# Kernel tuning notes

Measured on AMD Instinct MI355X. Metric: run time of the kernel, lower is better.

## Reference

```python
import jax, jax.numpy as jnp
import numpy as np
import math

HIDDEN = 128

def setup_inputs() -> dict:
    key = jax.random.key(0)
    k1, k2, k3 = jax.random.split(key, 3)
    X = jax.random.normal(k1, (4, 4096, HIDDEN), dtype=jnp.float32)
    # nn.Linear(hidden, 3*hidden): weight [3H, H], bias [3H]
    bound = 1.0 / math.sqrt(HIDDEN)
    W = jax.random.uniform(k2, (3 * HIDDEN, HIDDEN), minval=-bound, maxval=bound, dtype=jnp.float32)
    b = jax.random.uniform(k3, (3 * HIDDEN,), minval=-bound, maxval=bound, dtype=jnp.float32)
    return {"X": X, "W": W, "b": b}

def reference(X, W, b):
    H = X.shape[-1]
    # fused QKV projection: X @ W^T + b -> [B, S, 3H]
    qkv = jnp.einsum('bsh,oh->bso', X, W) + b
    Q, K, V = jnp.split(qkv, 3, axis=-1)
    # scaled dot-product attention (single head)
    scores = jnp.einsum('bqh,bkh->bqk', Q, K) / jnp.sqrt(jnp.asarray(H, X.dtype))
    weights = jax.nn.softmax(scores, axis=-1)
    return jnp.einsum('bqk,bkh->bqh', weights, V)
```

## Files before the change

kernel.cpp:

```cpp
#include <hip/hip_runtime.h>
#include <hip/hip_fp16.h>

typedef _Float16 f16;
typedef __attribute__((ext_vector_type(8))) _Float16 f16x8;
typedef __attribute__((ext_vector_type(4))) float f32x4;
typedef __attribute__((ext_vector_type(4))) unsigned int u32x4;
typedef __attribute__((ext_vector_type(2))) unsigned int u32x2;

#define BB 4
#define SS 4096
#define HH 128
#define SC2 0.12752462157076558f
#define M2  5.7707801635558535f

union H2U { __half2 h; unsigned int u; };
union VU { u32x4 v; unsigned short s[8]; };
union F8U { u32x4 u; f16x8 h; };

__global__ __launch_bounds__(256, 2) void qkv_gemm(
    const float* __restrict__ X, const float* __restrict__ W,
    const float* __restrict__ bias, f16* __restrict__ Qh,
    f16* __restrict__ Kh, f16* __restrict__ Vh)
{
    const int bid = blockIdx.x;
    const int t = threadIdx.x;
    const int w = t >> 6, lane = t & 63;
    const int c = lane & 15, quad = lane >> 4;
    const int rbase = bid * 32;

    f16x8 wf[6][4];
#pragma unroll
    for (int mt = 0; mt < 6; ++mt) {
        const float* wr = W + (size_t)(w * 96 + mt * 16 + c) * HH + quad * 8;
#pragma unroll
        for (int kc = 0; kc < 4; ++kc) {
            float4 a = *(const float4*)(wr + kc * 32);
            float4 b = *(const float4*)(wr + kc * 32 + 4);
            H2U u0, u1, u2, u3;
            u0.h = __floats2half2_rn(a.x, a.y);
            u1.h = __floats2half2_rn(a.z, a.w);
            u2.h = __floats2half2_rn(b.x, b.y);
            u3.h = __floats2half2_rn(b.z, b.w);
            F8U pk; pk.u.x = u0.u; pk.u.y = u1.u; pk.u.z = u2.u; pk.u.w = u3.u;
            wf[mt][kc] = pk.h;
        }
    }
    float4 bb[6];
#pragma unroll
    for (int mt = 0; mt < 6; ++mt)
        bb[mt] = *(const float4*)&bias[w * 96 + mt * 16 + quad * 4];

#pragma unroll
    for (int nt = 0; nt < 2; ++nt) {
        f16x8 xf[4];
        const float* xr = X + (size_t)(rbase + nt * 16 + c) * HH + quad * 8;
#pragma unroll
        for (int kc = 0; kc < 4; ++kc) {
            float4 a = *(const float4*)(xr + kc * 32);
            float4 b = *(const float4*)(xr + kc * 32 + 4);
            H2U u0, u1, u2, u3;
            u0.h = __floats2half2_rn(a.x, a.y);
            u1.h = __floats2half2_rn(a.z, a.w);
            u2.h = __floats2half2_rn(b.x, b.y);
            u3.h = __floats2half2_rn(b.z, b.w);
            F8U pk; pk.u.x = u0.u; pk.u.y = u1.u; pk.u.z = u2.u; pk.u.w = u3.u;
            xf[kc] = pk.h;
        }
        f32x4 acc[6];
#pragma unroll
        for (int mt = 0; mt < 6; ++mt) acc[mt] = (f32x4)0.f;
#pragma unroll
        for (int kc = 0; kc < 4; ++kc)
#pragma unroll
            for (int mt = 0; mt < 6; ++mt)
                acc[mt] = __builtin_amdgcn_mfma_f32_16x16x32_f16(wf[mt][kc], xf[kc], acc[mt], 0, 0, 0);

        const int xrow = rbase + nt * 16 + c;
#pragma unroll
        for (int mt = 0; mt < 6; ++mt) {
            const int gcol = w * 96 + mt * 16;
            const int seg = gcol >> 7;
            const int cc = (gcol & 127) + quad * 4;
            f16* dst = (seg == 0) ? Qh : (seg == 1) ? Kh : Vh;
            H2U h0, h1;
            h0.h = __floats2half2_rn(acc[mt][0] + bb[mt].x, acc[mt][1] + bb[mt].y);
            h1.h = __floats2half2_rn(acc[mt][2] + bb[mt].z, acc[mt][3] + bb[mt].w);
            u32x2 pk; pk.x = h0.u; pk.y = h1.u;
            *(u32x2*)(dst + (size_t)xrow * HH + cc) = pk;
        }
    }
}

#define BM 128
#define BN 64
#define LK 136
#define LV 72
#define LP 40

__global__ __launch_bounds__(256, 2) void attn_mfma(
    const f16* __restrict__ Qh, const f16* __restrict__ Kh,
    const f16* __restrict__ Vh, float* __restrict__ out,
    float* __restrict__ Opart, float* __restrict__ l_arr, int nsplit)
{
    __shared__ f16 sK[BN * LK];
    __shared__ f16 sVt[HH * LV];
    __shared__ f16 sP[4][32 * LP];

    const int bid = blockIdx.x;
    const int split = bid >> 7;
    const int inner = bid & 127;
    const int batch = inner & 3;
    const int qtile = inner >> 2;
    const int t = threadIdx.x;
    const int w = t >> 6, lane = t & 63;
    const int c = lane & 15, quad = lane >> 4;

    const int s0 = (64 * split) / nsplit;
    const int s1 = (64 * (split + 1)) / nsplit;
    const int nst = s1 - s0;
    const int kstart = s0 * BN;

    const f16* Qb = Qh + (size_t)batch * SS * HH;
    const f16* Kb = Kh + (size_t)batch * SS * HH;
    const f16* Vb = Vh + (size_t)batch * SS * HH;
    const int qbase = qtile * BM + w * 32;

    f16x8 qf[2][4];
#pragma unroll
    for (int qt = 0; qt < 2; ++qt)
#pragma unroll
        for (int kc = 0; kc < 4; ++kc)
            qf[qt][kc] = *(const f16x8*)(Qb + (size_t)(qbase + qt * 16 + c) * HH + kc * 32 + quad * 8);

    const int kr = t >> 2, q4 = t & 3;
    const f16* kgp = Kb + (size_t)(kstart + kr) * HH + q4 * 32;
    f16* ksp = sK + kr * LK + q4 * 32;
    const int vkp = t & 31, vhq = t >> 5;
    const f16* vgp = Vb + (size_t)(kstart + 2 * vkp) * HH + vhq * 16;

    u32x4 kbuf[4], vb0[2], vb1[2];
#pragma unroll
    for (int i = 0; i < 4; ++i) kbuf[i] = *(const u32x4*)(kgp + i * 8);
#pragma unroll
    for (int i = 0; i < 2; ++i) {
        vb0[i] = *(const u32x4*)(vgp + i * 8);
        vb1[i] = *(const u32x4*)(vgp + HH + i * 8);
    }

    f32x4 oacc[2][8];
#pragma unroll
    for (int mt = 0; mt < 2; ++mt)
#pragma unroll
        for (int nt = 0; nt < 8; ++nt) oacc[mt][nt] = (f32x4)0.f;
    f32x4 oaccl[2];
    oaccl[0] = (f32x4)0.f; oaccl[1] = (f32x4)0.f;
    const f16x8 ones = {1, 1, 1, 1, 1, 1, 1, 1};

    for (int st = 0; st < nst; ++st) {
        __syncthreads();
#pragma unroll
        for (int i = 0; i < 4; ++i) *(u32x4*)(ksp + i * 8) = kbuf[i];
        {
            VU a0, a1, b0, b1;
            a0.v = vb0[0]; a1.v = vb0[1]; b0.v = vb1[0]; b1.v = vb1[1];
#pragma unroll
            for (int d = 0; d < 8; ++d) {
                unsigned int pk = (unsigned int)a0.s[d] | ((unsigned int)b0.s[d] << 16);
                *(unsigned int*)&sVt[(vhq * 16 + d) * LV + 2 * vkp] = pk;
            }
#pragma unroll
            for (int d = 0; d < 8; ++d) {
                unsigned int pk = (unsigned int)a1.s[d] | ((unsigned int)b1.s[d] << 16);
                *(unsigned int*)&sVt[(vhq * 16 + 8 + d) * LV + 2 * vkp] = pk;
            }
        }
        __syncthreads();
        if (st + 1 < nst) {
            const f16* kg = kgp + (size_t)(st + 1) * BN * HH;
#pragma unroll
            for (int i = 0; i < 4; ++i) kbuf[i] = *(const u32x4*)(kg + i * 8);
            const f16* vg = vgp + (size_t)(st + 1) * BN * HH;
#pragma unroll
            for (int i = 0; i < 2; ++i) {
                vb0[i] = *(const u32x4*)(vg + i * 8);
                vb1[i] = *(const u32x4*)(vg + HH + i * 8);
            }
        }

        f32x4 sacc[4][2];
#pragma unroll
        for (int km = 0; km < 4; ++km)
#pragma unroll
            for (int qt = 0; qt < 2; ++qt) sacc[km][qt] = (f32x4)0.f;
#pragma unroll
        for (int kc = 0; kc < 4; ++kc) {
#pragma unroll
            for (int km = 0; km < 4; ++km) {
                f16x8 kf = *(const f16x8*)&sK[(km * 16 + c) * LK + kc * 32 + quad * 8];
#pragma unroll
                for (int qt = 0; qt < 2; ++qt)
                    sacc[km][qt] = __builtin_amdgcn_mfma_f32_16x16x32_f16(kf, qf[qt][kc], sacc[km][qt], 0, 0, 0);
            }
        }

#pragma unroll
        for (int h = 0; h < 2; ++h) {
#pragma unroll
            for (int qt = 0; qt < 2; ++qt) {
#pragma unroll
                for (int km2 = 0; km2 < 2; ++km2) {
                    const int km = 2 * h + km2;
                    float p0 = exp2f(sacc[km][qt][0] * SC2 - M2);
                    float p1 = exp2f(sacc[km][qt][1] * SC2 - M2);
                    float p2 = exp2f(sacc[km][qt][2] * SC2 - M2);
                    float p3 = exp2f(sacc[km][qt][3] * SC2 - M2);
                    H2U u0, u1;
                    u0.h = __floats2half2_rn(p0, p1);
                    u1.h = __floats2half2_rn(p2, p3);
                    u32x2 pk; pk.x = u0.u; pk.y = u1.u;
                    *(u32x2*)&sP[w][(qt * 16 + c) * LP + km2 * 16 + quad * 4] = pk;
                }
            }
            f16x8 pf[2];
#pragma unroll
            for (int mt = 0; mt < 2; ++mt)
                pf[mt] = *(const f16x8*)&sP[w][(mt * 16 + c) * LP + quad * 8];
#pragma unroll
            for (int mt = 0; mt < 2; ++mt)
                oaccl[mt] = __builtin_amdgcn_mfma_f32_16x16x32_f16(pf[mt], ones, oaccl[mt], 0, 0, 0);
#pragma unroll
            for (int nt = 0; nt < 8; ++nt) {
                f16x8 vf = *(const f16x8*)&sVt[(nt * 16 + c) * LV + h * 32 + quad * 8];
#pragma unroll
                for (int mt = 0; mt < 2; ++mt)
                    oacc[mt][nt] = __builtin_amdgcn_mfma_f32_16x16x32_f16(pf[mt], vf, oacc[mt][nt], 0, 0, 0);
            }
        }
    }

    float* Ob = (split == 0) ? out : (Opart + (size_t)(split - 1) * BB * SS * HH);
    float* ob = Ob + (size_t)(batch * SS + qbase) * HH;
    if (nsplit == 1) {
#pragma unroll
        for (int mt = 0; mt < 2; ++mt) {
#pragma unroll
            for (int r = 0; r < 4; ++r) {
                const float lv = 1.f / oaccl[mt][r];
                const int row = mt * 16 + quad * 4 + r;
#pragma unroll
                for (int nt = 0; nt < 8; ++nt)
                    ob[(size_t)row * HH + nt * 16 + c] = oacc[mt][nt][r] * lv;
            }
        }
    } else {
#pragma unroll
        for (int mt = 0; mt < 2; ++mt) {
#pragma unroll
            for (int r = 0; r < 4; ++r) {
                const int row = mt * 16 + quad * 4 + r;
#pragma unroll
                for (int nt = 0; nt < 8; ++nt)
                    ob[(size_t)row * HH + nt * 16 + c] = oacc[mt][nt][r];
            }
        }
        if (c == 0) {
#pragma unroll
            for (int mt = 0; mt < 2; ++mt)
#pragma unroll
                for (int r = 0; r < 4; ++r)
                    l_arr[((size_t)split * BB + batch) * SS + qbase + mt * 16 + quad * 4 + r] = oaccl[mt][r];
        }
    }
}

__global__ __launch_bounds__(256) void attn_merge(
    float* __restrict__ out, const float* __restrict__ Opart,
    const float* __restrict__ l_arr, int nsplit)
{
    const int idx = blockIdx.x * 256 + threadIdx.x;
    const int chunk = idx & 31;
    const int q = (idx >> 5) & (SS - 1);
    const int b = idx >> 17;
    float L = 0.f;
    for (int s = 0; s < nsplit; ++s)
        L += l_arr[((size_t)s * BB + b) * SS + q];
    float4 a = *(const float4*)(out + ((size_t)b * SS + q) * HH + chunk * 4);
    for (int s = 1; s < nsplit; ++s) {
        const float* Op = Opart + (size_t)(s - 1) * BB * SS * HH;
        float4 o = *(const float4*)(Op + ((size_t)b * SS + q) * HH + chunk * 4);
        a.x += o.x; a.y += o.y; a.z += o.z; a.w += o.w;
    }
    const float inv = 1.f / L;
    a.x *= inv; a.y *= inv; a.z *= inv; a.w *= inv;
    *(float4*)(out + ((size_t)b * SS + q) * HH + chunk * 4) = a;
}

extern "C" void kernel_launch(void* const* d_in, const int* in_sizes, int n_in,
                              void* d_out, int out_size, void* d_ws, size_t ws_size,
                              hipStream_t stream) {
    const float* X = (const float*)d_in[0];
    const float* W = (const float*)d_in[1];
    const float* bias = (const float*)d_in[2];
    float* out = (float*)d_out;

    char* ws = (char*)d_ws;
    const size_t qkv_bytes = (size_t)3 * BB * SS * HH * sizeof(f16);
    const size_t o_bytes   = (size_t)BB * SS * HH * sizeof(float);
    const size_t l_bytes   = (size_t)BB * SS * sizeof(float);

    int S = 1;
    for (int cand = 4; cand >= 2; --cand) {
        if (ws_size >= qkv_bytes + (size_t)(cand - 1) * o_bytes + (size_t)cand * l_bytes) {
            S = cand; break;
        }
    }

    f16* Qh = (f16*)ws;
    f16* Kh = Qh + (size_t)BB * SS * HH;
    f16* Vh = Kh + (size_t)BB * SS * HH;
    float* Opart = (float*)(ws + qkv_bytes);
    float* l_arr = (float*)(ws + qkv_bytes + (size_t)(S - 1) * o_bytes);

    qkv_gemm<<<512, 256, 0, stream>>>(X, W, bias, Qh, Kh, Vh);
    attn_mfma<<<128 * S, 256, 0, stream>>>(Qh, Kh, Vh, out, Opart, l_arr, S);
    if (S > 1)
        attn_merge<<<BB * SS * (HH / 4) / 256, 256, 0, stream>>>(out, Opart, l_arr, S);
}
```

Baseline: 133.6 us.

## Pre-convert W to fp16, double GEMM rows per block, load K fragments directly

Adds a small kernel that converts W to fp16 once per call, so each qkv_gemm block loads half-precision weights instead of converting fp32. Each GEMM block now covers 64 rows instead of 32, halving the grid and the per-block weight loads. The attention kernel drops the shared-memory K tile and reads K MFMA fragments straight from global memory each step, and the V transpose staging is reorganised into wider 4-key packed LDS writes. This costs an extra launch and higher register pressure from the 16 K fragments, and loses K reuse across waves through LDS.

```diff
diff --git a/kernel.cpp b/kernel.cpp
--- a/kernel.cpp
+++ b/kernel.cpp
@@ -17,8 +17,20 @@
 union VU { u32x4 v; unsigned short s[8]; };
 union F8U { u32x4 u; f16x8 h; };
 
+__global__ __launch_bounds__(256) void wcvt(const float* __restrict__ W,
+                                            f16* __restrict__ Wh)
+{
+    const int idx = (blockIdx.x * 256 + threadIdx.x) * 4;
+    float4 v = *(const float4*)(W + idx);
+    H2U h0, h1;
+    h0.h = __floats2half2_rn(v.x, v.y);
+    h1.h = __floats2half2_rn(v.z, v.w);
+    u32x2 pk; pk.x = h0.u; pk.y = h1.u;
+    *(u32x2*)(Wh + idx) = pk;
+}
+
 __global__ __launch_bounds__(256, 2) void qkv_gemm(
-    const float* __restrict__ X, const float* __restrict__ W,
+    const float* __restrict__ X, const f16* __restrict__ Wh,
     const float* __restrict__ bias, f16* __restrict__ Qh,
     f16* __restrict__ Kh, f16* __restrict__ Vh)
 {
@@ -26,24 +38,15 @@
     const int t = threadIdx.x;
     const int w = t >> 6, lane = t & 63;
     const int c = lane & 15, quad = lane >> 4;
-    const int rbase = bid * 32;
+    const int rbase = bid * 64;
 
     f16x8 wf[6][4];
 #pragma unroll
     for (int mt = 0; mt < 6; ++mt) {
-        const float* wr = W + (size_t)(w * 96 + mt * 16 + c) * HH + quad * 8;
-#pragma unroll
-        for (int kc = 0; kc < 4; ++kc) {
-            float4 a = *(const float4*)(wr + kc * 32);
-            float4 b = *(const float4*)(wr + kc * 32 + 4);
-            H2U u0, u1, u2, u3;
-            u0.h = __floats2half2_rn(a.x, a.y);
-            u1.h = __floats2half2_rn(a.z, a.w);
-            u2.h = __floats2half2_rn(b.x, b.y);
-            u3.h = __floats2half2_rn(b.z, b.w);
-            F8U pk; pk.u.x = u0.u; pk.u.y = u1.u; pk.u.z = u2.u; pk.u.w = u3.u;
-            wf[mt][kc] = pk.h;
-        }
+        const f16* wr = Wh + (size_t)(w * 96 + mt * 16 + c) * HH + quad * 8;
+#pragma unroll
+        for (int kc = 0; kc < 4; ++kc)
+            wf[mt][kc] = *(const f16x8*)(wr + kc * 32);
     }
     float4 bb[6];
 #pragma unroll
@@ -51,7 +54,7 @@
         bb[mt] = *(const float4*)&bias[w * 96 + mt * 16 + quad * 4];
 
 #pragma unroll
-    for (int nt = 0; nt < 2; ++nt) {
+    for (int nt = 0; nt < 4; ++nt) {
         f16x8 xf[4];
         const float* xr = X + (size_t)(rbase + nt * 16 + c) * HH + quad * 8;
 #pragma unroll
@@ -93,7 +96,6 @@
 
 #define BM 128
 #define BN 64
-#define LK 136
 #define LV 72
 #define LP 40
 
@@ -102,7 +104,6 @@
     const f16* __restrict__ Vh, float* __restrict__ out,
     float* __restrict__ Opart, float* __restrict__ l_arr, int nsplit)
 {
-    __shared__ f16 sK[BN * LK];
     __shared__ f16 sVt[HH * LV];
     __shared__ f16 sP[4][32 * LP];
 
@@ -132,20 +133,15 @@
         for (int kc = 0; kc < 4; ++kc)
             qf[qt][kc] = *(const f16x8*)(Qb + (size_t)(qbase + qt * 16 + c) * HH + kc * 32 + quad * 8);
 
-    const int kr = t >> 2, q4 = t & 3;
-    const f16* kgp = Kb + (size_t)(kstart + kr) * HH + q4 * 32;
-    f16* ksp = sK + kr * LK + q4 * 32;
-    const int vkp = t & 31, vhq = t >> 5;
-    const f16* vgp = Vb + (size_t)(kstart + 2 * vkp) * HH + vhq * 16;
-
-    u32x4 kbuf[4], vb0[2], vb1[2];
-#pragma unroll
-    for (int i = 0; i < 4; ++i) kbuf[i] = *(const u32x4*)(kgp + i * 8);
-#pragma unroll
-    for (int i = 0; i < 2; ++i) {
-        vb0[i] = *(const u32x4*)(vgp + i * 8);
-        vb1[i] = *(const u32x4*)(vgp + HH + i * 8);
-    }
+    const int vk4 = t & 15;
+    const int vdg = t >> 4;
+    const f16* vgp = Vb + (size_t)(kstart + 4 * vk4) * HH + vdg * 8;
+
+    u32x4 vb[4];
+#pragma unroll
+    for (int j = 0; j < 4; ++j) vb[j] = *(const u32x4*)(vgp + (size_t)j * HH);
+
+    const f16* kfb = Kb + (size_t)(kstart + c) * HH + quad * 8;
 
     f32x4 oacc[2][8];
 #pragma unroll
@@ -157,34 +153,31 @@
     const f16x8 ones = {1, 1, 1, 1, 1, 1, 1, 1};
 
     for (int st = 0; st < nst; ++st) {
+        const f16* kst = kfb + (size_t)st * BN * HH;
+        f16x8 kf[4][4];
+#pragma unroll
+        for (int km = 0; km < 4; ++km)
+#pragma unroll
+            for (int kc = 0; kc < 4; ++kc)
+                kf[km][kc] = *(const f16x8*)(kst + (size_t)(km * 16) * HH + kc * 32);
+
         __syncthreads();
-#pragma unroll
-        for (int i = 0; i < 4; ++i) *(u32x4*)(ksp + i * 8) = kbuf[i];
         {
-            VU a0, a1, b0, b1;
-            a0.v = vb0[0]; a1.v = vb0[1]; b0.v = vb1[0]; b1.v = vb1[1];
+            VU u0, u1, u2, u3;
+            u0.v = vb[0]; u1.v = vb[1]; u2.v = vb[2]; u3.v = vb[3];
 #pragma unroll
             for (int d = 0; d < 8; ++d) {
-                unsigned int pk = (unsigned int)a0.s[d] | ((unsigned int)b0.s[d] << 16);
-                *(unsigned int*)&sVt[(vhq * 16 + d) * LV + 2 * vkp] = pk;
-            }
-#pragma unroll
-            for (int d = 0; d < 8; ++d) {
-                unsigned int pk = (unsigned int)a1.s[d] | ((unsigned int)b1.s[d] << 16);
-                *(unsigned int*)&sVt[(vhq * 16 + 8 + d) * LV + 2 * vkp] = pk;
+                u32x2 pk;
+                pk.x = (unsigned int)u0.s[d] | ((unsigned int)u1.s[d] << 16);
+                pk.y = (unsigned int)u2.s[d] | ((unsigned int)u3.s[d] << 16);
+                *(u32x2*)&sVt[(vdg * 8 + d) * LV + 4 * vk4] = pk;
             }
         }
         __syncthreads();
         if (st + 1 < nst) {
-            const f16* kg = kgp + (size_t)(st + 1) * BN * HH;
-#pragma unroll
-            for (int i = 0; i < 4; ++i) kbuf[i] = *(const u32x4*)(kg + i * 8);
             const f16* vg = vgp + (size_t)(st + 1) * BN * HH;
 #pragma unroll
-            for (int i = 0; i < 2; ++i) {
-                vb0[i] = *(const u32x4*)(vg + i * 8);
-                vb1[i] = *(const u32x4*)(vg + HH + i * 8);
-            }
+            for (int j = 0; j < 4; ++j) vb[j] = *(const u32x4*)(vg + (size_t)j * HH);
         }
 
         f32x4 sacc[4][2];
@@ -193,15 +186,12 @@
 #pragma unroll
             for (int qt = 0; qt < 2; ++qt) sacc[km][qt] = (f32x4)0.f;
 #pragma unroll
-        for (int kc = 0; kc < 4; ++kc) {
-#pragma unroll
-            for (int km = 0; km < 4; ++km) {
-                f16x8 kf = *(const f16x8*)&sK[(km * 16 + c) * LK + kc * 32 + quad * 8];
+        for (int kc = 0; kc < 4; ++kc)
+#pragma unroll
+            for (int km = 0; km < 4; ++km)
 #pragma unroll
                 for (int qt = 0; qt < 2; ++qt)
-                    sacc[km][qt] = __builtin_amdgcn_mfma_f32_16x16x32_f16(kf, qf[qt][kc], sacc[km][qt], 0, 0, 0);
-            }
-        }
+                    sacc[km][qt] = __builtin_amdgcn_mfma_f32_16x16x32_f16(kf[km][kc], qf[qt][kc], sacc[km][qt], 0, 0, 0);
 
 #pragma unroll
         for (int h = 0; h < 2; ++h) {
@@ -305,12 +295,13 @@
 
     char* ws = (char*)d_ws;
     const size_t qkv_bytes = (size_t)3 * BB * SS * HH * sizeof(f16);
+    const size_t wh_bytes  = (size_t)384 * HH * sizeof(f16);
     const size_t o_bytes   = (size_t)BB * SS * HH * sizeof(float);
     const size_t l_bytes   = (size_t)BB * SS * sizeof(float);
 
     int S = 1;
     for (int cand = 4; cand >= 2; --cand) {
-        if (ws_size >= qkv_bytes + (size_t)(cand - 1) * o_bytes + (size_t)cand * l_bytes) {
+        if (ws_size >= qkv_bytes + wh_bytes + (size_t)(cand - 1) * o_bytes + (size_t)cand * l_bytes) {
             S = cand; break;
         }
     }
@@ -318,10 +309,12 @@
     f16* Qh = (f16*)ws;
     f16* Kh = Qh + (size_t)BB * SS * HH;
     f16* Vh = Kh + (size_t)BB * SS * HH;
-    float* Opart = (float*)(ws + qkv_bytes);
-    float* l_arr = (float*)(ws + qkv_bytes + (size_t)(S - 1) * o_bytes);
-
-    qkv_gemm<<<512, 256, 0, stream>>>(X, W, bias, Qh, Kh, Vh);
+    f16* Wh = (f16*)(ws + qkv_bytes);
+    float* Opart = (float*)(ws + qkv_bytes + wh_bytes);
+    float* l_arr = (float*)(ws + qkv_bytes + wh_bytes + (size_t)(S - 1) * o_bytes);
+
+    wcvt<<<48, 256, 0, stream>>>(W, Wh);
+    qkv_gemm<<<256, 256, 0, stream>>>(X, Wh, bias, Qh, Kh, Vh);
     attn_mfma<<<128 * S, 256, 0, stream>>>(Qh, Kh, Vh, out, Opart, l_arr, S);
     if (S > 1)
         attn_merge<<<BB * SS * (HH / 4) / 256, 256, 0, stream>>>(out, Opart, l_arr, S);
```

New measurement: 159.0 us. 18.9% more time.
